# Kernel tuning notes

Hardware: AMD Instinct MI355X
Metric: run time of the kernel (lower is better)

Reference implementation:

```python
import jax, jax.numpy as jnp
import numpy as np

N_NODES = 10000
N_EDGES = 160000
N_GRAPHS = 16
IN_FEAT = 128
DIMS = [(128, 512), (512, 256), (256, 64), (64, 32)]


def _lin_params(key, fin, fout):
    w = jax.random.normal(key, (fin, fout), jnp.float32) * (1.0 / np.sqrt(fin))
    b = jnp.zeros((fout,), jnp.float32)
    return w, b


def setup_inputs() -> dict:
    key = jax.random.key(0)
    ks = jax.random.split(key, 64)
    inp = {}
    inp['x'] = jax.random.normal(ks[0], (N_NODES, IN_FEAT), jnp.float32)
    inp['edge_index'] = jax.random.randint(ks[1], (2, N_EDGES), 0, N_NODES, jnp.int64 if jax.config.jax_enable_x64 else jnp.int32)
    inp['batch'] = jnp.sort(jax.random.randint(ks[2], (N_NODES,), 0, N_GRAPHS))
    ki = 3
    for li, (fin, fout) in enumerate(DIMS, start=1):
        for nm in ['q', 'k', 'v', 's']:
            w, b = _lin_params(ks[ki], fin, fout); ki += 1
            inp[f'W{nm}{li}'] = w
            inp[f'b{nm}{li}'] = b
    inp['Wg'], inp['bg'] = _lin_params(ks[ki], 32, 1); ki += 1
    inp['Wf'], inp['bf'] = _lin_params(ks[ki], 32, 9)
    return inp


def _segment_softmax(logits, seg, num_segments):
    m = jax.ops.segment_max(logits, seg, num_segments=num_segments)
    e = jnp.exp(logits - m[seg])
    s = jax.ops.segment_sum(e, seg, num_segments=num_segments)
    return e / s[seg]


def _transformer_conv(x, src, dst, Wq, bq, Wk, bk, Wv, bv, Ws, bs):
    # PyG TransformerConv, heads=1: attention over incoming edges per dst node.
    n = x.shape[0]
    q = x @ Wq + bq
    k = x @ Wk + bk
    v = x @ Wv + bv
    d = q.shape[-1]
    logits = jnp.sum(q[dst] * k[src], axis=-1) / jnp.sqrt(jnp.asarray(d, x.dtype))
    alpha = _segment_softmax(logits, dst, n)  # [E]
    agg = jax.ops.segment_sum(alpha[:, None] * v[src], dst, num_segments=n)
    return agg + (x @ Ws + bs)  # root/skip connection


def reference(x, edge_index, batch,
              Wq1, bq1, Wk1, bk1, Wv1, bv1, Ws1, bs1,
              Wq2, bq2, Wk2, bk2, Wv2, bv2, Ws2, bs2,
              Wq3, bq3, Wk3, bk3, Wv3, bv3, Ws3, bs3,
              Wq4, bq4, Wk4, bk4, Wv4, bv4, Ws4, bs4,
              Wg, bg, Wf, bf):
    src, dst = edge_index[0], edge_index[1]
    layers = [
        (Wq1, bq1, Wk1, bk1, Wv1, bv1, Ws1, bs1),
        (Wq2, bq2, Wk2, bk2, Wv2, bv2, Ws2, bs2),
        (Wq3, bq3, Wk3, bk3, Wv3, bv3, Ws3, bs3),
        (Wq4, bq4, Wk4, bk4, Wv4, bv4, Ws4, bs4),
    ]
    h = x
    for p in layers:
        h = jax.nn.elu(_transformer_conv(h, src, dst, *p))
    # GlobalAttention pooling: gate softmax per graph, weighted sum.
    gate = (h @ Wg + bg)[:, 0]  # [N]
    a = _segment_softmax(gate, batch, N_GRAPHS)
    pooled = jax.ops.segment_sum(a[:, None] * h, batch, num_segments=N_GRAPHS)  # [G, 32]
    return pooled @ Wf + bf  # [G, 9]
```

## Files before the change

### kernel.cpp

```cpp
#include <hip/hip_runtime.h>
#include <hip/hip_bf16.h>
#include <math.h>


typedef __bf16 bf16x8 __attribute__((ext_vector_type(8)));
typedef __bf16 bf16x4 __attribute__((ext_vector_type(4)));
typedef float f32x4 __attribute__((ext_vector_type(4)));

#define GBM 128
#define GBN 128
#define GBK 64

#if __has_builtin(__builtin_amdgcn_global_load_lds)
#define ASYNC_LDS 1
__device__ __forceinline__ void gload16(const __bf16* g, __bf16* l) {
  __builtin_amdgcn_global_load_lds(
      (const __attribute__((address_space(1))) unsigned int*)g,
      (__attribute__((address_space(3))) unsigned int*)l, 16, 0, 0);
}
#endif

__global__ __launch_bounds__(256) void gemm_mfma_kernel(
    const __bf16* __restrict__ A, const __bf16* __restrict__ Bt,
    const float* __restrict__ bias, __bf16* __restrict__ qkvs,
    int M, int K, int Nc) {
  __shared__ __bf16 As[GBM * 64];
  __shared__ __bf16 Bs[GBN * 64];
  const int tid = threadIdx.x;
  const int wave = tid >> 6;
  const int lane = tid & 63;
  const int quad = lane >> 4;
  const int l16 = lane & 15;
  const int m0 = blockIdx.y * GBM;
  const int n0 = blockIdx.x * GBN;
  const int wm = (wave & 1) * 64;
  const int wn = (wave >> 1) * 64;

  const int r8 = lane >> 3;
  const int sseg = lane & 7;

  f32x4 acc[4][4] = {};

  for (int k0 = 0; k0 < K; k0 += GBK) {
#pragma unroll
    for (int it = 0; it < 4; ++it) {
      const int rbase = wave * 32 + it * 8;
      const int row = rbase + r8;
      const int sw = sseg ^ r8;
      const __bf16* ga = A + (size_t)(m0 + row) * K + k0 + sw * 8;
      const __bf16* gb = Bt + (size_t)(n0 + row) * K + k0 + sw * 8;
#ifdef ASYNC_LDS
      gload16(ga, As + rbase * 64);
      gload16(gb, Bs + rbase * 64);
#else
      *(bf16x8*)(As + row * 64 + sseg * 8) = *(const bf16x8*)ga;
      *(bf16x8*)(Bs + row * 64 + sseg * 8) = *(const bf16x8*)gb;
#endif
    }
    __syncthreads();

#pragma unroll
    for (int ks = 0; ks < 2; ++ks) {
      bf16x8 af[4], bfr[4];
#pragma unroll
      for (int i = 0; i < 4; ++i) {
        const int ra = wm + i * 16 + l16;
        const int rb = wn + i * 16 + l16;
        const int ps = ((ks * 4 + quad) ^ (l16 & 7)) * 8;
        af[i]  = *(const bf16x8*)(As + ra * 64 + ps);
        bfr[i] = *(const bf16x8*)(Bs + rb * 64 + ps);
      }
#pragma unroll
      for (int mi = 0; mi < 4; ++mi)
#pragma unroll
        for (int ni = 0; ni < 4; ++ni)
          acc[mi][ni] = __builtin_amdgcn_mfma_f32_16x16x32_bf16(
              af[mi], bfr[ni], acc[mi][ni], 0, 0, 0);
    }
    __syncthreads();
  }

  float bsv[4];
#pragma unroll
  for (int ni = 0; ni < 4; ++ni) bsv[ni] = bias[n0 + wn + ni * 16 + l16];
#pragma unroll
  for (int mi = 0; mi < 4; ++mi) {
#pragma unroll
    for (int r = 0; r < 4; ++r) {
      int row = m0 + wm + mi * 16 + quad * 4 + r;
      if (row < M) {
        size_t rb = (size_t)row * Nc;
#pragma unroll
        for (int ni = 0; ni < 4; ++ni) {
          int col = n0 + wn + ni * 16 + l16;
          qkvs[rb + col] = (__bf16)(acc[mi][ni][r] + bsv[ni]);
        }
      }
    }
  }
}

#define WTOT 860160
#define BTOT 3456
#define XTOT 320000
__global__ void pack_all_kernel(
    const float* W0q, const float* W0k, const float* W0v, const float* W0s,
    const float* b0q, const float* b0k, const float* b0v, const float* b0s,
    const float* W1q, const float* W1k, const float* W1v, const float* W1s,
    const float* b1q, const float* b1k, const float* b1v, const float* b1s,
    const float* W2q, const float* W2k, const float* W2v, const float* W2s,
    const float* b2q, const float* b2k, const float* b2v, const float* b2s,
    const float* W3q, const float* W3k, const float* W3v, const float* W3s,
    const float* b3q, const float* b3k, const float* b3v, const float* b3s,
    const float* __restrict__ x, __bf16* __restrict__ xb,
    __bf16* __restrict__ Wt, float* __restrict__ bcat) {
  const int t = blockIdx.x * 256 + threadIdx.x;
  if (t < WTOT) {
    int l, local, ksh, fsh;
    if (t < 262144)      { l = 0; local = t;          ksh = 7; fsh = 9; }
    else if (t < 786432) { l = 1; local = t - 262144; ksh = 9; fsh = 8; }
    else if (t < 851968) { l = 2; local = t - 786432; ksh = 8; fsh = 6; }
    else                 { l = 3; local = t - 851968; ksh = 6; fsh = 5; }
    const int K = 1 << ksh, fout = 1 << fsh;
    int c = local >> ksh;
    int kk = local & (K - 1);
    int blk = c >> fsh;
    int j = c & (fout - 1);
    const float* W;
    if (l == 0)      W = blk == 0 ? W0q : blk == 1 ? W0k : blk == 2 ? W0v : W0s;
    else if (l == 1) W = blk == 0 ? W1q : blk == 1 ? W1k : blk == 2 ? W1v : W1s;
    else if (l == 2) W = blk == 0 ? W2q : blk == 1 ? W2k : blk == 2 ? W2v : W2s;
    else             W = blk == 0 ? W3q : blk == 1 ? W3k : blk == 2 ? W3v : W3s;
    Wt[t] = (__bf16)W[((size_t)kk << fsh) + j];
  } else if (t < WTOT + BTOT) {
    int u = t - WTOT;
    int l, local, fsh, boff;
    if (u < 2048)      { l = 0; local = u;        fsh = 9; boff = 0; }
    else if (u < 3072) { l = 1; local = u - 2048; fsh = 8; boff = 2048; }
    else if (u < 3328) { l = 2; local = u - 3072; fsh = 6; boff = 3072; }
    else               { l = 3; local = u - 3328; fsh = 5; boff = 3328; }
    const int fout = 1 << fsh;
    int blk = local >> fsh, j = local & (fout - 1);
    const float* b;
    if (l == 0)      b = blk == 0 ? b0q : blk == 1 ? b0k : blk == 2 ? b0v : b0s;
    else if (l == 1) b = blk == 0 ? b1q : blk == 1 ? b1k : blk == 2 ? b1v : b1s;
    else if (l == 2) b = blk == 0 ? b2q : blk == 1 ? b2k : blk == 2 ? b2v : b2s;
    else             b = blk == 0 ? b3q : blk == 1 ? b3k : blk == 2 ? b3v : b3s;
    bcat[boff + local] = b[j];
  } else if (t < WTOT + BTOT + XTOT) {
    int i = t - (WTOT + BTOT);
    float4 v = ((const float4*)x)[i];
    bf16x4 o;
    o[0] = (__bf16)v.x; o[1] = (__bf16)v.y; o[2] = (__bf16)v.z; o[3] = (__bf16)v.w;
    *(bf16x4*)(xb + (size_t)i * 4) = o;
  }
}

__global__ void hist_kernel(const int* __restrict__ dst, int* __restrict__ deg, int E) {
  int e = blockIdx.x * blockDim.x + threadIdx.x;
  if (e < E) atomicAdd(&deg[dst[e]], 1);
}

__global__ __launch_bounds__(1024) void scan_kernel(const int* __restrict__ deg,
                                                    int* __restrict__ offs, int N) {
  __shared__ int sums[1024];
  const int tid = threadIdx.x;
  const int chunk = (N + 1023) / 1024;
  const int start = tid * chunk;
  int s = 0;
  for (int i = 0; i < chunk; ++i) {
    int idx = start + i;
    if (idx < N) s += deg[idx];
  }
  sums[tid] = s;
  __syncthreads();
  for (int off = 1; off < 1024; off <<= 1) {
    int t = (tid >= off) ? sums[tid - off] : 0;
    __syncthreads();
    sums[tid] += t;
    __syncthreads();
  }
  int run = (tid == 0) ? 0 : sums[tid - 1];
  for (int i = 0; i < chunk; ++i) {
    int idx = start + i;
    if (idx < N) {
      offs[idx] = run;
      run += deg[idx];
    }
  }
  if (tid == 1023) offs[N] = sums[1023];
}

__global__ void scatter_kernel(const int* __restrict__ src, const int* __restrict__ dst,
                               const int* __restrict__ offs, int* __restrict__ cursor,
                               int* __restrict__ csr_src, int* __restrict__ csr_dst, int E) {
  int e = blockIdx.x * blockDim.x + threadIdx.x;
  if (e >= E) return;
  int d = dst[e];
  int pos = offs[d] + atomicAdd(&cursor[d], 1);
  csr_src[pos] = src[e];
  csr_dst[pos] = d;
}

__global__ __launch_bounds__(256) void edge_logit_kernel(
    const __bf16* __restrict__ qkvs, const int* __restrict__ csr_src,
    const int* __restrict__ csr_dst, float* __restrict__ logits,
    int E, int d, float scale, int lpe_log2) {
  const int t = blockIdx.x * 256 + threadIdx.x;
  const int g = t >> lpe_log2;
  const int lpe = 1 << lpe_log2;
  const int l = t & (lpe - 1);
  if (g >= E) return;
  const int ld = 4 * d;
  const int s = csr_src[g];
  const int dt = csr_dst[g];
  const __bf16* qr = qkvs + (size_t)dt * ld;
  const __bf16* kr = qkvs + (size_t)s * ld + d;
  const int n8 = d >> 3;
  float p = 0.f;
  for (int i = l; i < n8; i += lpe) {
    bf16x8 qv = *(const bf16x8*)(qr + i * 8);
    bf16x8 kv = *(const bf16x8*)(kr + i * 8);
#pragma unroll
    for (int j = 0; j < 8; ++j) p += (float)qv[j] * (float)kv[j];
  }
  for (int off = lpe >> 1; off; off >>= 1) p += __shfl_xor(p, off);
  if (l == 0) logits[g] = p * scale;
}

__global__ __launch_bounds__(256) void node_softmax_kernel(
    const int* __restrict__ offs, float* __restrict__ logits, int N) {
  const int node = (blockIdx.x * 256 + threadIdx.x) >> 6;
  const int lane = threadIdx.x & 63;
  if (node >= N) return;
  const int begin = offs[node];
  const int deg = offs[node + 1] - begin;
  if (deg == 0) return;
  float m = -INFINITY;
  for (int i = lane; i < deg; i += 64) m = fmaxf(m, logits[begin + i]);
#pragma unroll
  for (int off = 32; off; off >>= 1) m = fmaxf(m, __shfl_xor(m, off));
  float ss = 0.f;
  for (int i = lane; i < deg; i += 64) ss += __expf(logits[begin + i] - m);
#pragma unroll
  for (int off = 32; off; off >>= 1) ss += __shfl_xor(ss, off);
  const float inv = 1.0f / ss;
  for (int i = lane; i < deg; i += 64)
    logits[begin + i] = __expf(logits[begin + i] - m) * inv;
}

__global__ __launch_bounds__(256) void attn_agg_kernel(
    const __bf16* __restrict__ qkvs, const int* __restrict__ csr_src,
    const int* __restrict__ offs, const float* __restrict__ logits,
    __bf16* __restrict__ h_out, int N, int d, int segs_log2, int lpg_log2,
    const float* __restrict__ Wg, const float* __restrict__ bg,
    float* __restrict__ gate_out) {
  const int W = (blockIdx.x * 256 + threadIdx.x) >> 6;
  const int lane = threadIdx.x & 63;
  const int node = W >> segs_log2;
  const int seg = W & ((1 << segs_log2) - 1);
  if (node >= N) return;
  const int lpg = 1 << lpg_log2;
  const int ng = 64 >> lpg_log2;
  const int g = lane >> lpg_log2;
  const int l = lane & (lpg - 1);
  const int f0 = seg * (lpg << 3) + l * 8;
  const int ld = 4 * d;
  const int begin = offs[node];
  const int deg = offs[node + 1] - begin;

  float acc[8] = {0.f, 0.f, 0.f, 0.f, 0.f, 0.f, 0.f, 0.f};
  const __bf16* vbase = qkvs + 2 * (size_t)d;

#pragma unroll 2
  for (int i = g; i < deg; i += ng) {
    int pos = begin + i;
    float w = logits[pos];
    int s = csr_src[pos];
    bf16x8 vv = *(const bf16x8*)(vbase + (size_t)s * ld + f0);
#pragma unroll
    for (int j = 0; j < 8; ++j) acc[j] += w * (float)vv[j];
  }

  for (int off = lpg; off < 64; off <<= 1) {
#pragma unroll
    for (int j = 0; j < 8; ++j) acc[j] += __shfl_xor(acc[j], off);
  }

  float rr[8];
  bf16x8 sk = *(const bf16x8*)(qkvs + (size_t)node * ld + 3 * d + f0);
  bf16x8 o;
#pragma unroll
  for (int j = 0; j < 8; ++j) {
    float r = acc[j] + (float)sk[j];
    r = (r > 0.f) ? r : expm1f(r);
    rr[j] = r;
    o[j] = (__bf16)r;
  }
  *(bf16x8*)(h_out + (size_t)node * d + f0) = o;

  if (gate_out) {
    float gp = 0.f;
#pragma unroll
    for (int j = 0; j < 8; ++j) gp += rr[j] * Wg[f0 + j];
    for (int off = 1; off < lpg; off <<= 1) gp += __shfl_xor(gp, off);
    if (lane == 0) gate_out[node] = gp + bg[0];
  }
}

__global__ __launch_bounds__(256) void pool_final_kernel(
    const __bf16* __restrict__ h, const float* __restrict__ gate,
    const int* __restrict__ batch, int N, const float* __restrict__ Wf,
    const float* __restrict__ bf_, float* __restrict__ out) {
  __shared__ float red[256];
  __shared__ float pooled_s[32];
  __shared__ float m_s, inv_s;
  __shared__ int sb[2];
  const int g = blockIdx.x;
  const int tid = threadIdx.x;

  if (tid < 2) {
    int target = g + tid;
    int lo = 0, hi = N;
    while (lo < hi) {
      int mid = (lo + hi) >> 1;
      if (batch[mid] < target) lo = mid + 1;
      else hi = mid;
    }
    sb[tid] = lo;
  }
  __syncthreads();
  const int s = sb[0];
  const int e_end = sb[1];

  float m = -INFINITY;
  for (int i = s + tid; i < e_end; i += 256) m = fmaxf(m, gate[i]);
  red[tid] = m;
  __syncthreads();
  for (int off = 128; off; off >>= 1) {
    if (tid < off) red[tid] = fmaxf(red[tid], red[tid + off]);
    __syncthreads();
  }
  if (tid == 0) m_s = red[0];
  __syncthreads();
  m = m_s;

  float ss = 0.f;
  for (int i = s + tid; i < e_end; i += 256) ss += __expf(gate[i] - m);
  red[tid] = ss;
  __syncthreads();
  for (int off = 128; off; off >>= 1) {
    if (tid < off) red[tid] += red[tid + off];
    __syncthreads();
  }
  if (tid == 0) inv_s = (e_end > s) ? (1.0f / red[0]) : 0.f;
  __syncthreads();
  const float inv = inv_s;

  const int f = tid & 31;
  const int grp = tid >> 5;
  float acc = 0.f;
  for (int i = s + grp; i < e_end; i += 8)
    acc += __expf(gate[i] - m) * (float)h[(size_t)i * 32 + f];
  red[tid] = acc;
  __syncthreads();
  if (tid < 32) {
    float a = 0.f;
#pragma unroll
    for (int j = 0; j < 8; ++j) a += red[j * 32 + tid];
    pooled_s[tid] = a * inv;
  }
  __syncthreads();

  if (tid < 9) {
    float o = bf_[tid];
#pragma unroll
    for (int kk = 0; kk < 32; ++kk) o += pooled_s[kk] * Wf[kk * 9 + tid];
    out[g * 9 + tid] = o;
  }
}

extern "C" void kernel_launch(void* const* d_in, const int* in_sizes, int n_in,
                              void* d_out, int out_size, void* d_ws, size_t ws_size,
                              hipStream_t stream) {
  const int N = in_sizes[2];
  const int E = in_sizes[1] / 2;
  const int G = 16;
  const int NP = N + 128;

  const float* x = (const float*)d_in[0];
  const int* ei = (const int*)d_in[1];
  const int* batch = (const int*)d_in[2];
  const int* src = ei;
  const int* dst = ei + E;
  const float* Wg = (const float*)d_in[35];
  const float* bg = (const float*)d_in[36];
  const float* Wf = (const float*)d_in[37];
  const float* bf_ = (const float*)d_in[38];
  float* out = (float*)d_out;

  char* p = (char*)d_ws;
  auto carve = [&](size_t bytes) -> char* {
    char* r = p;
    p += (bytes + 255) & ~(size_t)255;
    return r;
  };
  int* deg = (int*)carve((size_t)2 * N * 4);
  int* cursor = deg + N;
  int* offs = (int*)carve((size_t)(N + 1) * 4);
  int* csr_src = (int*)carve((size_t)E * 4);
  int* csr_dst = (int*)carve((size_t)E * 4);
  float* logits = (float*)carve((size_t)E * 4);
  __bf16* Ab = (__bf16*)carve((size_t)NP * 128 * 2);
  __bf16* Wt = (__bf16*)carve((size_t)WTOT * 2);
  float* bcat = (float*)carve(BTOT * 4);
  __bf16* qkvs = (__bf16*)carve((size_t)N * 2048 * 2);
  __bf16* ha = (__bf16*)carve((size_t)NP * 512 * 2);
  __bf16* hb = (__bf16*)carve((size_t)NP * 512 * 2);
  float* gate = (float*)carve((size_t)N * 4);
  (void)ws_size;

  hipMemsetAsync(deg, 0, (size_t)2 * N * 4, stream);
  hist_kernel<<<(E + 255) / 256, 256, 0, stream>>>(dst, deg, E);
  scan_kernel<<<1, 1024, 0, stream>>>(deg, offs, N);
  scatter_kernel<<<(E + 255) / 256, 256, 0, stream>>>(src, dst, offs, cursor, csr_src, csr_dst, E);

  const float** di = (const float**)d_in;
  pack_all_kernel<<<(WTOT + BTOT + XTOT + 255) / 256, 256, 0, stream>>>(
      di[3], di[5], di[7], di[9], di[4], di[6], di[8], di[10],
      di[11], di[13], di[15], di[17], di[12], di[14], di[16], di[18],
      di[19], di[21], di[23], di[25], di[20], di[22], di[24], di[26],
      di[27], di[29], di[31], di[33], di[28], di[30], di[32], di[34],
      x, Ab, Wt, bcat);

  const int fins[4] = {128, 512, 256, 64};
  const int fouts[4] = {512, 256, 64, 32};
  const size_t woffs[4] = {0, 262144, 786432, 851968};
  const int boffs[4] = {0, 2048, 3072, 3328};
  const __bf16* hin = Ab;
  __bf16* houts[4] = {ha, hb, ha, hb};

  for (int l = 0; l < 4; ++l) {
    const int fin = fins[l], fout = fouts[l];
    const int Nc = 4 * fout;
    __bf16* hout = houts[l];

    dim3 grid(Nc / GBN, (N + GBM - 1) / GBM);
    gemm_mfma_kernel<<<grid, 256, 0, stream>>>(hin, Wt + woffs[l], bcat + boffs[l],
                                               qkvs, N, fin, Nc);

    float scale = 1.0f / sqrtf((float)fout);
    int lpe_log2 = (fout >= 128) ? 4 : (fout == 64 ? 3 : 2);
    size_t lthreads = (size_t)E << lpe_log2;
    edge_logit_kernel<<<(lthreads + 255) / 256, 256, 0, stream>>>(
        qkvs, csr_src, csr_dst, logits, E, fout, scale, lpe_log2);

    node_softmax_kernel<<<((size_t)N * 64 + 255) / 256, 256, 0, stream>>>(
        offs, logits, N);

    int lpg_log2 = (fout >= 128) ? 4 : (fout == 64 ? 3 : 2);
    int fs = 8 << lpg_log2;
    int segs_log2 = 0;
    while ((fs << segs_log2) < fout) ++segs_log2;
    size_t waves = (size_t)N << segs_log2;
    const bool last = (l == 3);
    attn_agg_kernel<<<(waves * 64 + 255) / 256, 256, 0, stream>>>(
        qkvs, csr_src, offs, logits, hout, N, fout, segs_log2, lpg_log2,
        last ? Wg : nullptr, last ? bg : nullptr, last ? gate : nullptr);
    hin = hout;
  }

  pool_final_kernel<<<G, 256, 0, stream>>>(hin, gate, batch, N, Wf, bf_, out);
}
```

Baseline: 370.9 us.

## Fuse edge logits, softmax and aggregation into one online-softmax kernel

Replaces the three per-layer kernels (edge logit, node softmax, attention aggregation) with a single templated kernel that handles one destination node per wave. The query row is held in registers, and logits are computed and consumed on the fly with an online-softmax rescale, so the logits array and the csr_dst array are no longer needed. This removes two launches per layer and the global round-trips of the logits. In exchange, one wave now covers all feature columns of a node, which means larger register arrays for D=512 and less parallelism per node than the earlier split into feature segments.

```diff
diff --git a/kernel.cpp b/kernel.cpp
--- a/kernel.cpp
+++ b/kernel.cpp
@@ -193,118 +193,125 @@
 
 __global__ void scatter_kernel(const int* __restrict__ src, const int* __restrict__ dst,
                                const int* __restrict__ offs, int* __restrict__ cursor,
-                               int* __restrict__ csr_src, int* __restrict__ csr_dst, int E) {
+                               int* __restrict__ csr_src, int E) {
   int e = blockIdx.x * blockDim.x + threadIdx.x;
   if (e >= E) return;
   int d = dst[e];
   int pos = offs[d] + atomicAdd(&cursor[d], 1);
   csr_src[pos] = src[e];
-  csr_dst[pos] = d;
-}
-
-__global__ __launch_bounds__(256) void edge_logit_kernel(
+}
+
+template <int D, int LPG_LOG2, bool GATE>
+__global__ __launch_bounds__(256) void attn_fused_kernel(
     const __bf16* __restrict__ qkvs, const int* __restrict__ csr_src,
-    const int* __restrict__ csr_dst, float* __restrict__ logits,
-    int E, int d, float scale, int lpe_log2) {
-  const int t = blockIdx.x * 256 + threadIdx.x;
-  const int g = t >> lpe_log2;
-  const int lpe = 1 << lpe_log2;
-  const int l = t & (lpe - 1);
-  if (g >= E) return;
-  const int ld = 4 * d;
-  const int s = csr_src[g];
-  const int dt = csr_dst[g];
-  const __bf16* qr = qkvs + (size_t)dt * ld;
-  const __bf16* kr = qkvs + (size_t)s * ld + d;
-  const int n8 = d >> 3;
-  float p = 0.f;
-  for (int i = l; i < n8; i += lpe) {
-    bf16x8 qv = *(const bf16x8*)(qr + i * 8);
-    bf16x8 kv = *(const bf16x8*)(kr + i * 8);
-#pragma unroll
-    for (int j = 0; j < 8; ++j) p += (float)qv[j] * (float)kv[j];
-  }
-  for (int off = lpe >> 1; off; off >>= 1) p += __shfl_xor(p, off);
-  if (l == 0) logits[g] = p * scale;
-}
-
-__global__ __launch_bounds__(256) void node_softmax_kernel(
-    const int* __restrict__ offs, float* __restrict__ logits, int N) {
+    const int* __restrict__ offs, __bf16* __restrict__ h_out, int N,
+    float scale, const float* __restrict__ Wg, const float* __restrict__ bg,
+    float* __restrict__ gate_out) {
+  constexpr int LPG = 1 << LPG_LOG2;
+  constexpr int NG = 64 / LPG;
+  constexpr int NIT = D / (8 * LPG);
+  constexpr int LD = 4 * D;
   const int node = (blockIdx.x * 256 + threadIdx.x) >> 6;
   const int lane = threadIdx.x & 63;
   if (node >= N) return;
+  const int g = lane >> LPG_LOG2;
+  const int l = lane & (LPG - 1);
   const int begin = offs[node];
   const int deg = offs[node + 1] - begin;
-  if (deg == 0) return;
+
+  const __bf16* qrow = qkvs + (size_t)node * LD;
+  bf16x8 qreg[NIT];
+#pragma unroll
+  for (int it = 0; it < NIT; ++it)
+    qreg[it] = *(const bf16x8*)(qrow + it * LPG * 8 + l * 8);
+
   float m = -INFINITY;
-  for (int i = lane; i < deg; i += 64) m = fmaxf(m, logits[begin + i]);
-#pragma unroll
-  for (int off = 32; off; off >>= 1) m = fmaxf(m, __shfl_xor(m, off));
-  float ss = 0.f;
-  for (int i = lane; i < deg; i += 64) ss += __expf(logits[begin + i] - m);
-#pragma unroll
-  for (int off = 32; off; off >>= 1) ss += __shfl_xor(ss, off);
-  const float inv = 1.0f / ss;
-  for (int i = lane; i < deg; i += 64)
-    logits[begin + i] = __expf(logits[begin + i] - m) * inv;
-}
-
-__global__ __launch_bounds__(256) void attn_agg_kernel(
-    const __bf16* __restrict__ qkvs, const int* __restrict__ csr_src,
-    const int* __restrict__ offs, const float* __restrict__ logits,
-    __bf16* __restrict__ h_out, int N, int d, int segs_log2, int lpg_log2,
-    const float* __restrict__ Wg, const float* __restrict__ bg,
-    float* __restrict__ gate_out) {
-  const int W = (blockIdx.x * 256 + threadIdx.x) >> 6;
-  const int lane = threadIdx.x & 63;
-  const int node = W >> segs_log2;
-  const int seg = W & ((1 << segs_log2) - 1);
-  if (node >= N) return;
-  const int lpg = 1 << lpg_log2;
-  const int ng = 64 >> lpg_log2;
-  const int g = lane >> lpg_log2;
-  const int l = lane & (lpg - 1);
-  const int f0 = seg * (lpg << 3) + l * 8;
-  const int ld = 4 * d;
-  const int begin = offs[node];
-  const int deg = offs[node + 1] - begin;
-
-  float acc[8] = {0.f, 0.f, 0.f, 0.f, 0.f, 0.f, 0.f, 0.f};
-  const __bf16* vbase = qkvs + 2 * (size_t)d;
-
-#pragma unroll 2
-  for (int i = g; i < deg; i += ng) {
-    int pos = begin + i;
-    float w = logits[pos];
-    int s = csr_src[pos];
-    bf16x8 vv = *(const bf16x8*)(vbase + (size_t)s * ld + f0);
-#pragma unroll
-    for (int j = 0; j < 8; ++j) acc[j] += w * (float)vv[j];
-  }
-
-  for (int off = lpg; off < 64; off <<= 1) {
-#pragma unroll
-    for (int j = 0; j < 8; ++j) acc[j] += __shfl_xor(acc[j], off);
-  }
-
-  float rr[8];
-  bf16x8 sk = *(const bf16x8*)(qkvs + (size_t)node * ld + 3 * d + f0);
-  bf16x8 o;
-#pragma unroll
-  for (int j = 0; j < 8; ++j) {
-    float r = acc[j] + (float)sk[j];
-    r = (r > 0.f) ? r : expm1f(r);
-    rr[j] = r;
-    o[j] = (__bf16)r;
-  }
-  *(bf16x8*)(h_out + (size_t)node * d + f0) = o;
-
-  if (gate_out) {
-    float gp = 0.f;
-#pragma unroll
-    for (int j = 0; j < 8; ++j) gp += rr[j] * Wg[f0 + j];
-    for (int off = 1; off < lpg; off <<= 1) gp += __shfl_xor(gp, off);
-    if (lane == 0) gate_out[node] = gp + bg[0];
+  float s = 0.f;
+  float acc[NIT][8] = {};
+
+  for (int base = 0; base < deg; base += NG) {
+    const int i = base + g;
+    const bool valid = i < deg;
+    int sidx = valid ? csr_src[begin + i] : 0;
+
+    float p = 0.f;
+    if (valid) {
+      const __bf16* krow = qkvs + (size_t)sidx * LD + D;
+      bf16x8 kv[NIT];
+#pragma unroll
+      for (int it = 0; it < NIT; ++it)
+        kv[it] = *(const bf16x8*)(krow + it * LPG * 8 + l * 8);
+#pragma unroll
+      for (int it = 0; it < NIT; ++it)
+#pragma unroll
+        for (int j = 0; j < 8; ++j) p += (float)qreg[it][j] * (float)kv[it][j];
+    }
+#pragma unroll
+    for (int off = LPG >> 1; off; off >>= 1) p += __shfl_xor(p, off);
+    const float logit = valid ? p * scale : -INFINITY;
+
+    float cmax = logit;
+#pragma unroll
+    for (int off = LPG; off < 64; off <<= 1)
+      cmax = fmaxf(cmax, __shfl_xor(cmax, off));
+    const float m_new = fmaxf(m, cmax);
+    const float alpha = __expf(m - m_new);
+    s *= alpha;
+#pragma unroll
+    for (int it = 0; it < NIT; ++it)
+#pragma unroll
+      for (int j = 0; j < 8; ++j) acc[it][j] *= alpha;
+    const float w = __expf(logit - m_new);
+    s += w;
+    m = m_new;
+
+    if (valid) {
+      const __bf16* vrow = qkvs + (size_t)sidx * LD + 2 * D;
+      bf16x8 vv[NIT];
+#pragma unroll
+      for (int it = 0; it < NIT; ++it)
+        vv[it] = *(const bf16x8*)(vrow + it * LPG * 8 + l * 8);
+#pragma unroll
+      for (int it = 0; it < NIT; ++it)
+#pragma unroll
+        for (int j = 0; j < 8; ++j) acc[it][j] += w * (float)vv[it][j];
+    }
+  }
+
+#pragma unroll
+  for (int off = LPG; off < 64; off <<= 1) {
+    s += __shfl_xor(s, off);
+#pragma unroll
+    for (int it = 0; it < NIT; ++it)
+#pragma unroll
+      for (int j = 0; j < 8; ++j) acc[it][j] += __shfl_xor(acc[it][j], off);
+  }
+  const float inv = (deg > 0) ? (1.0f / s) : 0.f;
+
+  if (g == 0) {
+    float rr[NIT][8];
+#pragma unroll
+    for (int it = 0; it < NIT; ++it) {
+      const int f0 = it * LPG * 8 + l * 8;
+      bf16x8 sk = *(const bf16x8*)(qrow + 3 * D + f0);
+      bf16x8 o;
+#pragma unroll
+      for (int j = 0; j < 8; ++j) {
+        float r = acc[it][j] * inv + (float)sk[j];
+        r = (r > 0.f) ? r : expm1f(r);
+        rr[it][j] = r;
+        o[j] = (__bf16)r;
+      }
+      *(bf16x8*)(h_out + (size_t)node * D + f0) = o;
+    }
+    if (GATE) {
+      float gp = 0.f;
+#pragma unroll
+      for (int j = 0; j < 8; ++j) gp += rr[0][j] * Wg[l * 8 + j];
+#pragma unroll
+      for (int off = 1; off < LPG; off <<= 1) gp += __shfl_xor(gp, off);
+      if (l == 0) gate_out[node] = gp + bg[0];
+    }
   }
 }
 
@@ -409,8 +416,6 @@
   int* cursor = deg + N;
   int* offs = (int*)carve((size_t)(N + 1) * 4);
   int* csr_src = (int*)carve((size_t)E * 4);
-  int* csr_dst = (int*)carve((size_t)E * 4);
-  float* logits = (float*)carve((size_t)E * 4);
   __bf16* Ab = (__bf16*)carve((size_t)NP * 128 * 2);
   __bf16* Wt = (__bf16*)carve((size_t)WTOT * 2);
   float* bcat = (float*)carve(BTOT * 4);
@@ -423,7 +428,7 @@
   hipMemsetAsync(deg, 0, (size_t)2 * N * 4, stream);
   hist_kernel<<<(E + 255) / 256, 256, 0, stream>>>(dst, deg, E);
   scan_kernel<<<1, 1024, 0, stream>>>(deg, offs, N);
-  scatter_kernel<<<(E + 255) / 256, 256, 0, stream>>>(src, dst, offs, cursor, csr_src, csr_dst, E);
+  scatter_kernel<<<(E + 255) / 256, 256, 0, stream>>>(src, dst, offs, cursor, csr_src, E);
 
   const float** di = (const float**)d_in;
   pack_all_kernel<<<(WTOT + BTOT + XTOT + 255) / 256, 256, 0, stream>>>(
@@ -439,6 +444,7 @@
   const int boffs[4] = {0, 2048, 3072, 3328};
   const __bf16* hin = Ab;
   __bf16* houts[4] = {ha, hb, ha, hb};
+  const int agrid = ((size_t)N * 64 + 255) / 256;
 
   for (int l = 0; l < 4; ++l) {
     const int fin = fins[l], fout = fouts[l];
@@ -450,23 +456,19 @@
                                                qkvs, N, fin, Nc);
 
     float scale = 1.0f / sqrtf((float)fout);
-    int lpe_log2 = (fout >= 128) ? 4 : (fout == 64 ? 3 : 2);
-    size_t lthreads = (size_t)E << lpe_log2;
-    edge_logit_kernel<<<(lthreads + 255) / 256, 256, 0, stream>>>(
-        qkvs, csr_src, csr_dst, logits, E, fout, scale, lpe_log2);
-
-    node_softmax_kernel<<<((size_t)N * 64 + 255) / 256, 256, 0, stream>>>(
-        offs, logits, N);
-
-    int lpg_log2 = (fout >= 128) ? 4 : (fout == 64 ? 3 : 2);
-    int fs = 8 << lpg_log2;
-    int segs_log2 = 0;
-    while ((fs << segs_log2) < fout) ++segs_log2;
-    size_t waves = (size_t)N << segs_log2;
-    const bool last = (l == 3);
-    attn_agg_kernel<<<(waves * 64 + 255) / 256, 256, 0, stream>>>(
-        qkvs, csr_src, offs, logits, hout, N, fout, segs_log2, lpg_log2,
-        last ? Wg : nullptr, last ? bg : nullptr, last ? gate : nullptr);
+    if (l == 0) {
+      attn_fused_kernel<512, 4, false><<<agrid, 256, 0, stream>>>(
+          qkvs, csr_src, offs, hout, N, scale, nullptr, nullptr, nullptr);
+    } else if (l == 1) {
+      attn_fused_kernel<256, 4, false><<<agrid, 256, 0, stream>>>(
+          qkvs, csr_src, offs, hout, N, scale, nullptr, nullptr, nullptr);
+    } else if (l == 2) {
+      attn_fused_kernel<64, 3, false><<<agrid, 256, 0, stream>>>(
+          qkvs, csr_src, offs, hout, N, scale, nullptr, nullptr, nullptr);
+    } else {
+      attn_fused_kernel<32, 2, true><<<agrid, 256, 0, stream>>>(
+          qkvs, csr_src, offs, hout, N, scale, Wg, bg, gate);
+    }
     hin = hout;
   }
 
```

Measured after the change: 356.7 us. 1.04x faster.
